# Performance work log

Measured on AMD Instinct MI355X. Metric: run time of the kernel, lower is better.

Reference implementation:

```python
import jax, jax.numpy as jnp
import numpy as np

B, S, IN, E, H, NH = 32, 1024, 16, 128, 256, 4
DH = E // NH
EPS = 1e-5


def _ln(x, g, b):
    mu = jnp.mean(x, axis=-1, keepdims=True)
    var = jnp.mean(jnp.square(x - mu), axis=-1, keepdims=True)
    return (x - mu) * jax.lax.rsqrt(var + EPS) * g + b


def setup_inputs() -> dict:
    key = jax.random.key(0)
    ks = iter(jax.random.split(key, 32))
    n = lambda shape, s=0.02: jax.random.normal(next(ks), shape, jnp.float32) * s
    inp = {
        "x": jax.random.normal(next(ks), (B, S, IN), jnp.float32),
        "mask": jax.random.uniform(next(ks), (B, S), jnp.float32),
        "embed_w": n((E, IN)), "embed_b": jnp.zeros((E,), jnp.float32),
        # 3 encoder layers, params stacked on leading layer axis
        "in_proj_w": n((3, 3 * E, E)), "in_proj_b": jnp.zeros((3, 3 * E), jnp.float32),
        "out_w": n((3, E, E)), "out_b": jnp.zeros((3, E), jnp.float32),
        "ln1_g": jnp.ones((3, E), jnp.float32), "ln1_b": jnp.zeros((3, E), jnp.float32),
        "ln2_g": jnp.ones((3, E), jnp.float32), "ln2_b": jnp.zeros((3, E), jnp.float32),
        "ffn_w1": n((3, E, E)), "ffn_b1": jnp.zeros((3, E), jnp.float32),
        "ffn_w2": n((3, E, E)), "ffn_b2": jnp.zeros((3, E), jnp.float32),
        "cls_w1": n((H, E)), "cls_b1": jnp.zeros((H,), jnp.float32),
        "cls_w2": n((H, H)), "cls_b2": jnp.zeros((H,), jnp.float32),
        "cls_w3": n((H, H)), "cls_b3": jnp.zeros((H,), jnp.float32),
        "cls_w4": n((1, H)), "cls_b4": jnp.zeros((1,), jnp.float32),
    }
    return inp


def _encoder_layer(x, ipw, ipb, ow, ob, g1, b1, g2, b2, w1, fb1, w2, fb2):
    # PyTorch TransformerEncoderLayer, norm_first=False (post-norm), relu FFN
    qkv = x @ ipw.T + ipb                      # [B,S,3E]
    q, k, v = jnp.split(qkv, 3, axis=-1)
    q = q.reshape(B, S, NH, DH).transpose(0, 2, 1, 3)
    k = k.reshape(B, S, NH, DH).transpose(0, 2, 1, 3)
    v = v.reshape(B, S, NH, DH).transpose(0, 2, 1, 3)
    scores = jnp.einsum("bhqd,bhkd->bhqk", q, k) / np.sqrt(DH)  # naive O(S^2) math SDPA
    attn = jax.nn.softmax(scores, axis=-1)
    o = jnp.einsum("bhqk,bhkd->bhqd", attn, v)
    o = o.transpose(0, 2, 1, 3).reshape(B, S, E) @ ow.T + ob
    x = _ln(x + o, g1, b1)
    ff = jax.nn.relu(x @ w1.T + fb1) @ w2.T + fb2
    return _ln(x + ff, g2, b2)


def reference(x, mask, embed_w, embed_b, in_proj_w, in_proj_b, out_w, out_b,
              ln1_g, ln1_b, ln2_g, ln2_b, ffn_w1, ffn_b1, ffn_w2, ffn_b2,
              cls_w1, cls_b1, cls_w2, cls_b2, cls_w3, cls_b3, cls_w4, cls_b4):
    h = jax.nn.relu(x @ embed_w.T + embed_b)   # [B,S,E]
    for i in range(3):
        h = _encoder_layer(h, in_proj_w[i], in_proj_b[i], out_w[i], out_b[i],
                           ln1_g[i], ln1_b[i], ln2_g[i], ln2_b[i],
                           ffn_w1[i], ffn_b1[i], ffn_w2[i], ffn_b2[i])
    pooled = jnp.sum(h * mask[:, :, None], axis=1)  # [B,E] masked sum pool
    z = jax.nn.relu(pooled @ cls_w1.T + cls_b1)
    z = jax.nn.relu(z @ cls_w2.T + cls_b2)
    z = jax.nn.relu(z @ cls_w3.T + cls_b3)
    return jax.nn.sigmoid(z @ cls_w4.T + cls_b4)    # [B,1]
```

## Files before the change

### kernel.cpp

```cpp
#include <hip/hip_runtime.h>
#include <hip/hip_bf16.h>
#include <math.h>

#define B 32
#define S 1024
#define IN_DIM 16
#define E 128
#define NH 4
#define DH 32
#define HDIM 256
#define ROWS (B*S)
#define EPS 1e-5f

#define N_IPW (3*384*128)
#define N_SQ  (3*128*128)
#define NCVT ((N_IPW + 3*N_SQ) / 256)

typedef __bf16 bf16x8 __attribute__((ext_vector_type(8)));
typedef __bf16 bf16x4 __attribute__((ext_vector_type(4)));
typedef __bf16 bf16x2 __attribute__((ext_vector_type(2)));
typedef float f32x4 __attribute__((ext_vector_type(4)));
typedef float f32x16 __attribute__((ext_vector_type(16)));

#define MFMA16 __builtin_amdgcn_mfma_f32_16x16x32_bf16
#define MFMA32 __builtin_amdgcn_mfma_f32_32x32x16_bf16

union BF2U { bf16x2 b; unsigned int u; };
__device__ inline unsigned int pk2(float a, float b) {
    BF2U x; x.b[0] = (__bf16)a; x.b[1] = (__bf16)b; return x.u;
}

union U8 { bf16x8 v8; bf16x4 v4[2]; unsigned u4[4]; };
__device__ inline void st8(__bf16* p, bf16x8 v) {
    U8 u; u.v8 = v;
    *(bf16x4*)p = u.v4[0];
    *(bf16x4*)(p + 4) = u.v4[1];
}
__device__ inline bf16x8 ld8(const __bf16* p) {
    U8 u;
    u.v4[0] = *(const bf16x4*)p;
    u.v4[1] = *(const bf16x4*)(p + 4);
    return u.v8;
}

__global__ __launch_bounds__(256) void k_embedcvt(
        const float* __restrict__ ipw, const float* __restrict__ ow,
        const float* __restrict__ w1, const float* __restrict__ w2,
        __bf16* __restrict__ wbo,
        const float* __restrict__ x, const float* __restrict__ W,
        const float* __restrict__ bias, __bf16* __restrict__ hb)
{
    int t = threadIdx.x;
    if (blockIdx.x < NCVT) {
        int i = blockIdx.x * 256 + t;
        float v;
        if (i < N_IPW) v = ipw[i];
        else if (i < N_IPW + N_SQ) v = ow[i - N_IPW];
        else if (i < N_IPW + 2 * N_SQ) v = w1[i - N_IPW - N_SQ];
        else v = w2[i - N_IPW - 2 * N_SQ];
        wbo[i] = (__bf16)v;
        return;
    }
    int row0 = (blockIdx.x - NCVT) * 16;
    __shared__ float xs[16][16];
    xs[t >> 4][t & 15] = x[(row0 + (t >> 4)) * IN_DIM + (t & 15)];
    __syncthreads();
    int sub = t >> 7, tc = t & 127;
    float w[16];
#pragma unroll
    for (int i = 0; i < 16; ++i) w[i] = W[tc * 16 + i];
    float bb = bias[tc];
#pragma unroll
    for (int rr = 0; rr < 8; ++rr) {
        int lr = sub * 8 + rr;
        float acc = bb;
#pragma unroll
        for (int i = 0; i < 16; ++i) acc += xs[lr][i] * w[i];
        hb[(size_t)(row0 + lr) * E + tc] = (__bf16)fmaxf(acc, 0.f);
    }
}

__global__ __launch_bounds__(512, 2) void k_qkvattn(
        const __bf16* __restrict__ hb, const __bf16* __restrict__ Wip,
        const float* __restrict__ bip, __bf16* __restrict__ O)
{
    __shared__ __attribute__((aligned(16))) __bf16 Ksh[1024][36];
    __shared__ __attribute__((aligned(16))) __bf16 Vsh[32][1036];
    __shared__ float lscr[8][64];

    int t = threadIdx.x, lane = t & 63, wv = t >> 6;
    int l15 = lane & 15, quad = lane >> 4;
    int l31 = lane & 31, hi = lane >> 5;
    int lb = ((blockIdx.x & 7) << 5) | (blockIdx.x >> 3);
    int half = lb & 1, bh = lb >> 1;
    int hh = bh & 3, b = bh >> 2;

    const __bf16* hpanel = hb + (size_t)b * S * E;

    const float qscale = 0.1767766952966369f * 1.4426950408889634f * 8388608.0f;
    const float C2 = 1065101558.0f;
    f32x16 cinit16, z16;
#pragma unroll
    for (int i = 0; i < 16; ++i) { cinit16[i] = C2; z16[i] = 0.f; }

    bf16x8 bQ[2][2];
    {
        bf16x8 bWq[8];
#pragma unroll
        for (int ch = 0; ch < 8; ++ch)
            bWq[ch] = *(const bf16x8*)&Wip[(size_t)(hh*32 + l31)*128 + ch*16 + hi*8];
        float bq = bip[hh*32 + l31];
#pragma unroll
        for (int qt = 0; qt < 2; ++qt) {
            int qrow0 = half*512 + wv*64 + qt*32;
            f32x16 aq = z16;
#pragma unroll
            for (int ch = 0; ch < 8; ++ch) {
                bf16x8 ah = *(const bf16x8*)&hpanel[(size_t)(qrow0 + l31)*128 + ch*16 + hi*8];
                aq = MFMA32(ah, bWq[ch], aq, 0, 0, 0);
            }
            __bf16* PmS = &Ksh[wv*128 + qt*32][0];
#pragma unroll
            for (int r = 0; r < 16; ++r) {
                int q = (r & 3) + 8*(r >> 2) + 4*hi;
                PmS[q*36 + l31] = (__bf16)((aq[r] + bq) * qscale);
            }
        }
        __asm__ __volatile__("" ::: "memory");
#pragma unroll
        for (int qt = 0; qt < 2; ++qt) {
            const __bf16* PmS = &Ksh[wv*128 + qt*32][0];
            bQ[qt][0] = ld8(&PmS[l31*36 + hi*8]);
            bQ[qt][1] = ld8(&PmS[l31*36 + 16 + hi*8]);
        }
        __asm__ __volatile__("" ::: "memory");
    }
    __syncthreads();

    {
        bf16x8 bWk[2][4], bWv[2][4];
#pragma unroll
        for (int df = 0; df < 2; ++df)
#pragma unroll
            for (int kc = 0; kc < 4; ++kc) {
                bWk[df][kc] = *(const bf16x8*)&Wip[(size_t)(128 + hh*32 + df*16 + l15)*128 + kc*32 + quad*8];
                bWv[df][kc] = *(const bf16x8*)&Wip[(size_t)(256 + hh*32 + df*16 + l15)*128 + kc*32 + quad*8];
            }
        float bk0 = bip[128 + hh*32 + l15],  bk1 = bip[128 + hh*32 + 16 + l15];
        float bvb0 = bip[256 + hh*32 + l15], bvb1 = bip[256 + hh*32 + 16 + l15];
        int srow = wv*16 + l15;
        bf16x8 af[4], ag[4];
#pragma unroll
        for (int kc = 0; kc < 4; ++kc)
            af[kc] = *(const bf16x8*)&hpanel[(size_t)srow*128 + kc*32 + quad*8];
        const f32x4 z4 = {0.f, 0.f, 0.f, 0.f};
        for (int c = 0; c < 8; ++c) {
            if (c < 7) {
#pragma unroll
                for (int kc = 0; kc < 4; ++kc)
                    ag[kc] = *(const bf16x8*)&hpanel[(size_t)((c+1)*128 + srow)*128 + kc*32 + quad*8];
            }
            f32x4 k0 = z4, k1 = z4, v0 = z4, v1 = z4;
#pragma unroll
            for (int kc = 0; kc < 4; ++kc) {
                k0 = MFMA16(af[kc], bWk[0][kc], k0, 0, 0, 0);
                k1 = MFMA16(af[kc], bWk[1][kc], k1, 0, 0, 0);
                v0 = MFMA16(af[kc], bWv[0][kc], v0, 0, 0, 0);
                v1 = MFMA16(af[kc], bWv[1][kc], v1, 0, 0, 0);
            }
            int s0 = c*128 + wv*16 + quad*4;
#pragma unroll
            for (int r = 0; r < 4; ++r) {
                Ksh[s0 + r][l15]      = (__bf16)(k0[r] + bk0);
                Ksh[s0 + r][16 + l15] = (__bf16)(k1[r] + bk1);
            }
            uint2 u0, u1;
            u0.x = pk2(v0[0] + bvb0, v0[1] + bvb0);
            u0.y = pk2(v0[2] + bvb0, v0[3] + bvb0);
            u1.x = pk2(v1[0] + bvb1, v1[1] + bvb1);
            u1.y = pk2(v1[2] + bvb1, v1[3] + bvb1);
            *(uint2*)&Vsh[l15][s0] = u0;
            *(uint2*)&Vsh[16 + l15][s0] = u1;
#pragma unroll
            for (int kc = 0; kc < 4; ++kc) af[kc] = ag[kc];
        }
    }
    __syncthreads();

    f32x16 o[2];
    o[0] = z16; o[1] = z16;
    float lsum[2] = {0.f, 0.f};

    bf16x8 aK[2][2], bVf[4];
#pragma unroll
    for (int sub = 0; sub < 2; ++sub)
#pragma unroll
        for (int dh = 0; dh < 2; ++dh)
            aK[sub][dh] = ld8(&Ksh[sub*32 + l31][dh*16 + hi*8]);
#pragma unroll
    for (int ch = 0; ch < 4; ++ch) {
        U8 u;
        const __bf16* vp = &Vsh[l31][ch*16 + hi*4];
        u.v4[0] = *(const bf16x4*)vp;
        u.v4[1] = *(const bf16x4*)(vp + 8);
        bVf[ch] = u.v8;
    }

    for (int c = 0; c < 16; ++c) {
        bf16x8 aKn[2][2], bVn[4];
        if (c < 15) {
#pragma unroll
            for (int sub = 0; sub < 2; ++sub)
#pragma unroll
                for (int dh = 0; dh < 2; ++dh)
                    aKn[sub][dh] = ld8(&Ksh[(c+1)*64 + sub*32 + l31][dh*16 + hi*8]);
#pragma unroll
            for (int ch = 0; ch < 4; ++ch) {
                U8 u;
                const __bf16* vp = &Vsh[l31][(c+1)*64 + ch*16 + hi*4];
                u.v4[0] = *(const bf16x4*)vp;
                u.v4[1] = *(const bf16x4*)(vp + 8);
                bVn[ch] = u.v8;
            }
        }
#pragma unroll
        for (int qt = 0; qt < 2; ++qt) {
#pragma unroll
            for (int sub = 0; sub < 2; ++sub) {
                f32x16 acc = cinit16;
                acc = MFMA32(aK[sub][0], bQ[qt][0], acc, 0, 0, 0);
                acc = MFMA32(aK[sub][1], bQ[qt][1], acc, 0, 0, 0);
#pragma unroll
                for (int g = 0; g < 2; ++g) {
                    U8 u;
                    float ls = 0.f;
#pragma unroll
                    for (int r = 0; r < 4; ++r) {
                        int ia = (int)acc[g*8 + 2*r];
                        int ib = (int)acc[g*8 + 2*r + 1];
                        u.u4[r] = __builtin_amdgcn_perm((unsigned)ib, (unsigned)ia, 0x07060302u);
                        ls += __int_as_float(ia) + __int_as_float(ib);
                    }
                    lsum[qt] += ls;
                    o[qt] = MFMA32(u.v8, bVf[sub*2 + g], o[qt], 0, 0, 0);
                }
            }
        }
        if (c < 15) {
#pragma unroll
            for (int sub = 0; sub < 2; ++sub)
#pragma unroll
                for (int dh = 0; dh < 2; ++dh)
                    aK[sub][dh] = aKn[sub][dh];
#pragma unroll
            for (int ch = 0; ch < 4; ++ch) bVf[ch] = bVn[ch];
        }
    }

#pragma unroll
    for (int qt = 0; qt < 2; ++qt) {
        float ls = lsum[qt] + __shfl_xor(lsum[qt], 32);
        if (hi == 0) lscr[wv][qt*32 + l31] = 1.f / ls;
    }
    __asm__ __volatile__("" ::: "memory");
#pragma unroll
    for (int qt = 0; qt < 2; ++qt)
#pragma unroll
        for (int r = 0; r < 16; ++r) {
            int q = (r & 3) + 8*(r >> 2) + 4*hi;
            float li = lscr[wv][qt*32 + q];
            int row = half*512 + wv*64 + qt*32 + q;
            O[((size_t)(b * S) + row) * E + hh*32 + l31] = (__bf16)(o[qt][r] * li);
        }
}

__global__ __launch_bounds__(512, 2) void k_layer2(const __bf16* __restrict__ t0b,
        const __bf16* __restrict__ Wo, const float* __restrict__ ob,
        const float* __restrict__ g1, const float* __restrict__ bt1,
        const __bf16* __restrict__ W1, const float* __restrict__ b1v,
        const __bf16* __restrict__ W2, const float* __restrict__ b2v,
        const float* __restrict__ g2, const float* __restrict__ bt2,
        __bf16* __restrict__ hb)
{
    __shared__ __attribute__((aligned(16))) __bf16 As[64][132];
    __shared__ __attribute__((aligned(16))) __bf16 Ws[128][132];
    __shared__ float red[2][64][2];
    int t = threadIdx.x;
    int m0 = blockIdx.x * 64;
    int arow = t >> 3, acol = (t & 7) * 16;
    int wrow = t >> 2, wcol = (t & 3) * 32;
    {
        const __bf16* Ap = t0b + (size_t)(m0 + arow) * 128 + acol;
#pragma unroll
        for (int j = 0; j < 2; ++j)
            st8(&As[arow][acol + j * 8], *(const bf16x8*)&Ap[j * 8]);
        const __bf16* Wp = Wo + (size_t)wrow * 128 + wcol;
#pragma unroll
        for (int j = 0; j < 4; ++j)
            st8(&Ws[wrow][wcol + j * 8], *(const bf16x8*)&Wp[j * 8]);
    }
    __syncthreads();
    int lane = t & 63, wv = t >> 6;
    int l15 = lane & 15, quad = lane >> 4;
    int nh = wv & 1, mh = wv >> 1;
    f32x4 acc[4];

#pragma unroll
    for (int i = 0; i < 4; ++i) acc[i] = (f32x4){0.f, 0.f, 0.f, 0.f};
#pragma unroll
    for (int kc = 0; kc < 4; ++kc) {
        bf16x8 aw[4], ba;
#pragma unroll
        for (int nc = 0; nc < 4; ++nc)
            aw[nc] = ld8(&Ws[nh * 64 + nc * 16 + l15][kc * 32 + quad * 8]);
        ba = ld8(&As[mh * 16 + l15][kc * 32 + quad * 8]);
#pragma unroll
        for (int nc = 0; nc < 4; ++nc)
            acc[nc] = MFMA16(aw[nc], ba, acc[nc], 0, 0, 0);
    }
    float s1 = 0.f, s2 = 0.f;
    int m = m0 + mh * 16 + l15;
#pragma unroll
    for (int nc = 0; nc < 4; ++nc) {
        float4 bv = *(const float4*)&ob[nh * 64 + nc * 16 + quad * 4];
        bf16x4 rv = *(const bf16x4*)&hb[(size_t)m * 128 + nh * 64 + nc * 16 + quad * 4];
        acc[nc][0] += bv.x + (float)rv[0];
        acc[nc][1] += bv.y + (float)rv[1];
        acc[nc][2] += bv.z + (float)rv[2];
        acc[nc][3] += bv.w + (float)rv[3];
#pragma unroll
        for (int i = 0; i < 4; ++i) {
            s1 += acc[nc][i];
            s2 += acc[nc][i] * acc[nc][i];
        }
    }
    s1 += __shfl_xor(s1, 16); s1 += __shfl_xor(s1, 32);
    s2 += __shfl_xor(s2, 16); s2 += __shfl_xor(s2, 32);
    if (quad == 0) {
        red[nh][mh * 16 + l15][0] = s1;
        red[nh][mh * 16 + l15][1] = s2;
    }
    __syncthreads();
    float mu, rs;
    {
        int r = mh * 16 + l15;
        float S1 = red[0][r][0] + red[1][r][0];
        float S2 = red[0][r][1] + red[1][r][1];
        mu = S1 * (1.f / 128.f);
        float var = S2 * (1.f / 128.f) - mu * mu;
        rs = rsqrtf(var + EPS);
    }
    bf16x4 res2[4];
#pragma unroll
    for (int nc = 0; nc < 4; ++nc) {
        float4 gv = *(const float4*)&g1[nh * 64 + nc * 16 + quad * 4];
        float4 bb = *(const float4*)&bt1[nh * 64 + nc * 16 + quad * 4];
        float o0 = (acc[nc][0] - mu) * rs * gv.x + bb.x;
        float o1 = (acc[nc][1] - mu) * rs * gv.y + bb.y;
        float o2 = (acc[nc][2] - mu) * rs * gv.z + bb.z;
        float o3 = (acc[nc][3] - mu) * rs * gv.w + bb.w;
        bf16x4 xb;
        xb[0] = (__bf16)o0; xb[1] = (__bf16)o1;
        xb[2] = (__bf16)o2; xb[3] = (__bf16)o3;
        res2[nc] = xb;
        *(bf16x4*)&As[mh * 16 + l15][nh * 64 + nc * 16 + quad * 4] = xb;
    }
    {
        const __bf16* Wp = W1 + (size_t)wrow * 128 + wcol;
#pragma unroll
        for (int j = 0; j < 4; ++j)
            st8(&Ws[wrow][wcol + j * 8], *(const bf16x8*)&Wp[j * 8]);
    }
    __syncthreads();

#pragma unroll
    for (int i = 0; i < 4; ++i) acc[i] = (f32x4){0.f, 0.f, 0.f, 0.f};
#pragma unroll
    for (int kc = 0; kc < 4; ++kc) {
        bf16x8 aw[4], ba;
#pragma unroll
        for (int nc = 0; nc < 4; ++nc)
            aw[nc] = ld8(&Ws[nh * 64 + nc * 16 + l15][kc * 32 + quad * 8]);
        ba = ld8(&As[mh * 16 + l15][kc * 32 + quad * 8]);
#pragma unroll
        for (int nc = 0; nc < 4; ++nc)
            acc[nc] = MFMA16(aw[nc], ba, acc[nc], 0, 0, 0);
    }
    __syncthreads();
#pragma unroll
    for (int nc = 0; nc < 4; ++nc) {
        float4 bv = *(const float4*)&b1v[nh * 64 + nc * 16 + quad * 4];
        float v0 = fmaxf(acc[nc][0] + bv.x, 0.f);
        float v1 = fmaxf(acc[nc][1] + bv.y, 0.f);
        float v2 = fmaxf(acc[nc][2] + bv.z, 0.f);
        float v3 = fmaxf(acc[nc][3] + bv.w, 0.f);
        uint2 u; u.x = pk2(v0, v1); u.y = pk2(v2, v3);
        *(uint2*)&As[mh * 16 + l15][nh * 64 + nc * 16 + quad * 4] = u;
    }
    {
        const __bf16* Wp = W2 + (size_t)wrow * 128 + wcol;
#pragma unroll
        for (int j = 0; j < 4; ++j)
            st8(&Ws[wrow][wcol + j * 8], *(const bf16x8*)&Wp[j * 8]);
    }
    __syncthreads();

#pragma unroll
    for (int i = 0; i < 4; ++i) acc[i] = (f32x4){0.f, 0.f, 0.f, 0.f};
#pragma unroll
    for (int kc = 0; kc < 4; ++kc) {
        bf16x8 aw[4], ba;
#pragma unroll
        for (int nc = 0; nc < 4; ++nc)
            aw[nc] = ld8(&Ws[nh * 64 + nc * 16 + l15][kc * 32 + quad * 8]);
        ba = ld8(&As[mh * 16 + l15][kc * 32 + quad * 8]);
#pragma unroll
        for (int nc = 0; nc < 4; ++nc)
            acc[nc] = MFMA16(aw[nc], ba, acc[nc], 0, 0, 0);
    }
    s1 = 0.f; s2 = 0.f;
#pragma unroll
    for (int nc = 0; nc < 4; ++nc) {
        float4 bv = *(const float4*)&b2v[nh * 64 + nc * 16 + quad * 4];
        acc[nc][0] += bv.x + (float)res2[nc][0];
        acc[nc][1] += bv.y + (float)res2[nc][1];
        acc[nc][2] += bv.z + (float)res2[nc][2];
        acc[nc][3] += bv.w + (float)res2[nc][3];
#pragma unroll
        for (int i = 0; i < 4; ++i) {
            s1 += acc[nc][i];
            s2 += acc[nc][i] * acc[nc][i];
        }
    }
    s1 += __shfl_xor(s1, 16); s1 += __shfl_xor(s1, 32);
    s2 += __shfl_xor(s2, 16); s2 += __shfl_xor(s2, 32);
    if (quad == 0) {
        red[nh][mh * 16 + l15][0] = s1;
        red[nh][mh * 16 + l15][1] = s2;
    }
    __syncthreads();
    {
        int r = mh * 16 + l15;
        float S1 = red[0][r][0] + red[1][r][0];
        float S2 = red[0][r][1] + red[1][r][1];
        mu = S1 * (1.f / 128.f);
        float var = S2 * (1.f / 128.f) - mu * mu;
        rs = rsqrtf(var + EPS);
    }
#pragma unroll
    for (int nc = 0; nc < 4; ++nc) {
        float4 gv = *(const float4*)&g2[nh * 64 + nc * 16 + quad * 4];
        float4 bb = *(const float4*)&bt2[nh * 64 + nc * 16 + quad * 4];
        float o0 = (acc[nc][0] - mu) * rs * gv.x + bb.x;
        float o1 = (acc[nc][1] - mu) * rs * gv.y + bb.y;
        float o2 = (acc[nc][2] - mu) * rs * gv.z + bb.z;
        float o3 = (acc[nc][3] - mu) * rs * gv.w + bb.w;
        uint2 u; u.x = pk2(o0, o1); u.y = pk2(o2, o3);
        *(uint2*)&hb[(size_t)m * 128 + nh * 64 + nc * 16 + quad * 4] = u;
    }
}

__global__ __launch_bounds__(256) void k_pool1(const __bf16* __restrict__ h,
        const float* __restrict__ mask, float* __restrict__ part)
{
    int bx = blockIdx.x;
    int b = bx >> 3, ch = bx & 7, t = threadIdx.x;
    int sg = t >> 4, cg = t & 15;
    __shared__ float red[16][128];
    float acc[8];
#pragma unroll
    for (int j = 0; j < 8; ++j) acc[j] = 0.f;
    const __bf16* hp = h + ((size_t)(b * S + ch * 128 + sg)) * E + cg * 8;
    const float* mp = mask + b * S + ch * 128 + sg;
#pragma unroll
    for (int k = 0; k < 8; ++k) {
        float m = mp[k * 16];
        bf16x8 hv = *(const bf16x8*)&hp[(size_t)(k * 16) * E];
#pragma unroll
        for (int j = 0; j < 8; ++j) acc[j] += (float)hv[j] * m;
    }
#pragma unroll
    for (int j = 0; j < 8; ++j) red[sg][cg * 8 + j] = acc[j];
    __syncthreads();
    if (t < 128) {
        float a = 0.f;
#pragma unroll
        for (int sgi = 0; sgi < 16; ++sgi) a += red[sgi][t];
        part[(size_t)bx * E + t] = a;
    }
}

__global__ __launch_bounds__(256) void k_head(const float* __restrict__ part,
        const float* __restrict__ cw1, const float* __restrict__ cb1,
        const float* __restrict__ cw2, const float* __restrict__ cb2,
        const float* __restrict__ cw3, const float* __restrict__ cb3,
        const float* __restrict__ cw4, const float* __restrict__ cb4,
        float* __restrict__ out)
{
    int b = blockIdx.x, t = threadIdx.x;
    __shared__ float p[128], za[256], zb[256];
    __shared__ float red4[4];
    if (t < 128) {
        float a = 0.f;
#pragma unroll
        for (int c = 0; c < 8; ++c) a += part[(size_t)(b * 8 + c) * 128 + t];
        p[t] = a;
    }
    __syncthreads();
    float a1 = cb1[t];
    for (int k = 0; k < 128; ++k) a1 += p[k] * cw1[t * 128 + k];
    za[t] = fmaxf(a1, 0.f);
    __syncthreads();
    float a2 = cb2[t];
    for (int k = 0; k < 256; ++k) a2 += za[k] * cw2[t * 256 + k];
    zb[t] = fmaxf(a2, 0.f);
    __syncthreads();
    float a3 = cb3[t];
    for (int k = 0; k < 256; ++k) a3 += zb[k] * cw3[t * 256 + k];
    float z3 = fmaxf(a3, 0.f);
    float prt = z3 * cw4[t];
#pragma unroll
    for (int o2 = 32; o2; o2 >>= 1) prt += __shfl_xor(prt, o2);
    if ((t & 63) == 0) red4[t >> 6] = prt;
    __syncthreads();
    if (t == 0) {
        float sum = red4[0] + red4[1] + red4[2] + red4[3] + cb4[0];
        out[b] = 1.f / (1.f + __expf(-sum));
    }
}

extern "C" void kernel_launch(void* const* d_in, const int* in_sizes, int n_in,
                              void* d_out, int out_size, void* d_ws, size_t ws_size,
                              hipStream_t stream)
{
    const float* x     = (const float*)d_in[0];
    const float* mask  = (const float*)d_in[1];
    const float* emb_w = (const float*)d_in[2];
    const float* emb_b = (const float*)d_in[3];
    const float* ipw   = (const float*)d_in[4];
    const float* ipb   = (const float*)d_in[5];
    const float* ow    = (const float*)d_in[6];
    const float* ob    = (const float*)d_in[7];
    const float* ln1g  = (const float*)d_in[8];
    const float* ln1b  = (const float*)d_in[9];
    const float* ln2g  = (const float*)d_in[10];
    const float* ln2b  = (const float*)d_in[11];
    const float* w1    = (const float*)d_in[12];
    const float* fb1   = (const float*)d_in[13];
    const float* w2    = (const float*)d_in[14];
    const float* fb2   = (const float*)d_in[15];
    const float* cw1   = (const float*)d_in[16];
    const float* cb1   = (const float*)d_in[17];
    const float* cw2   = (const float*)d_in[18];
    const float* cb2   = (const float*)d_in[19];
    const float* cw3   = (const float*)d_in[20];
    const float* cb3   = (const float*)d_in[21];
    const float* cw4   = (const float*)d_in[22];
    const float* cb4   = (const float*)d_in[23];

    char* p = (char*)d_ws;
    __bf16* hb   = (__bf16*)p;   p += (size_t)ROWS * E * 2;
    p += (size_t)ROWS * 256 * 2;
    p += (size_t)ROWS * 32 * 4 * 2 / 4;
    __bf16* t0b  = (__bf16*)p;   p += (size_t)ROWS * E * 2;
    __bf16* wb   = (__bf16*)p;   p += (size_t)(N_IPW + 3 * N_SQ) * 2;
    float* part  = (float*)p;    p += (size_t)B * 8 * E * 4;

    __bf16* wb_ipw = wb;
    __bf16* wb_ow  = wb + N_IPW;
    __bf16* wb_w1  = wb_ow + N_SQ;
    __bf16* wb_w2  = wb_w1 + N_SQ;

    k_embedcvt<<<NCVT + ROWS / 16, 256, 0, stream>>>(
        ipw, ow, w1, w2, wb, x, emb_w, emb_b, hb);
    for (int L = 0; L < 3; ++L) {
        k_qkvattn<<<B * NH * 2, 512, 0, stream>>>(
            hb, wb_ipw + (size_t)L * 384 * 128, ipb + L * 384, t0b);
        k_layer2<<<ROWS / 64, 512, 0, stream>>>(
            t0b, wb_ow + (size_t)L * 128 * 128, ob + L * 128,
            ln1g + L * E, ln1b + L * E,
            wb_w1 + (size_t)L * 128 * 128, fb1 + L * 128,
            wb_w2 + (size_t)L * 128 * 128, fb2 + L * 128,
            ln2g + L * E, ln2b + L * E, hb);
    }
    k_pool1<<<B * 8, 256, 0, stream>>>(hb, mask, part);
    k_head<<<B, 256, 0, stream>>>(part, cw1, cb1, cw2, cb2, cw3, cb3, cw4, cb4,
                                  (float*)d_out);
}
```

Before: 296.5 us.

## Fuse masked pooling into final layer2 epilogue, vectorize head, stage embed weights

Removes the separate pooling kernel by computing masked per-block partial sums in the last layer's LayerNorm epilogue, using shuffles and shared memory, and writing 16 partials per batch. The head kernel now reduces 16 partials and uses float4 loads for its matvecs. The embed kernel stages the embedding weight in padded shared memory so global loads are coalesced. The aim is to save one launch and one re-read of the hidden state, at the cost of extra shuffles and a sync in layer2 on the final layer.

```diff
diff --git a/kernel.cpp b/kernel.cpp
--- a/kernel.cpp
+++ b/kernel.cpp
@@ -63,12 +63,18 @@
     }
     int row0 = (blockIdx.x - NCVT) * 16;
     __shared__ float xs[16][16];
+    __shared__ float wsh[128][17];
     xs[t >> 4][t & 15] = x[(row0 + (t >> 4)) * IN_DIM + (t & 15)];
+#pragma unroll
+    for (int j = 0; j < 8; ++j) {
+        int n = t * 8 + j;
+        wsh[n >> 4][n & 15] = W[n];
+    }
     __syncthreads();
     int sub = t >> 7, tc = t & 127;
     float w[16];
 #pragma unroll
-    for (int i = 0; i < 16; ++i) w[i] = W[tc * 16 + i];
+    for (int i = 0; i < 16; ++i) w[i] = wsh[tc][i];
     float bb = bias[tc];
 #pragma unroll
     for (int rr = 0; rr < 8; ++rr) {
@@ -280,11 +286,13 @@
         const __bf16* __restrict__ W1, const float* __restrict__ b1v,
         const __bf16* __restrict__ W2, const float* __restrict__ b2v,
         const float* __restrict__ g2, const float* __restrict__ bt2,
-        __bf16* __restrict__ hb)
+        __bf16* __restrict__ hb,
+        const float* __restrict__ mask, float* __restrict__ part, int doPool)
 {
     __shared__ __attribute__((aligned(16))) __bf16 As[64][132];
     __shared__ __attribute__((aligned(16))) __bf16 Ws[128][132];
     __shared__ float red[2][64][2];
+    __shared__ float psum[4][128];
     int t = threadIdx.x;
     int m0 = blockIdx.x * 64;
     int arow = t >> 3, acol = (t & 7) * 16;
@@ -447,6 +455,8 @@
         float var = S2 * (1.f / 128.f) - mu * mu;
         rs = rsqrtf(var + EPS);
     }
+    float pv[16];
+    float mk = doPool ? mask[m] : 0.f;
 #pragma unroll
     for (int nc = 0; nc < 4; ++nc) {
         float4 gv = *(const float4*)&g2[nh * 64 + nc * 16 + quad * 4];
@@ -457,36 +467,28 @@
         float o3 = (acc[nc][3] - mu) * rs * gv.w + bb.w;
         uint2 u; u.x = pk2(o0, o1); u.y = pk2(o2, o3);
         *(uint2*)&hb[(size_t)m * 128 + nh * 64 + nc * 16 + quad * 4] = u;
-    }
-}
-
-__global__ __launch_bounds__(256) void k_pool1(const __bf16* __restrict__ h,
-        const float* __restrict__ mask, float* __restrict__ part)
-{
-    int bx = blockIdx.x;
-    int b = bx >> 3, ch = bx & 7, t = threadIdx.x;
-    int sg = t >> 4, cg = t & 15;
-    __shared__ float red[16][128];
-    float acc[8];
-#pragma unroll
-    for (int j = 0; j < 8; ++j) acc[j] = 0.f;
-    const __bf16* hp = h + ((size_t)(b * S + ch * 128 + sg)) * E + cg * 8;
-    const float* mp = mask + b * S + ch * 128 + sg;
-#pragma unroll
-    for (int k = 0; k < 8; ++k) {
-        float m = mp[k * 16];
-        bf16x8 hv = *(const bf16x8*)&hp[(size_t)(k * 16) * E];
-#pragma unroll
-        for (int j = 0; j < 8; ++j) acc[j] += (float)hv[j] * m;
-    }
-#pragma unroll
-    for (int j = 0; j < 8; ++j) red[sg][cg * 8 + j] = acc[j];
-    __syncthreads();
-    if (t < 128) {
-        float a = 0.f;
-#pragma unroll
-        for (int sgi = 0; sgi < 16; ++sgi) a += red[sgi][t];
-        part[(size_t)bx * E + t] = a;
+        pv[nc*4 + 0] = o0 * mk; pv[nc*4 + 1] = o1 * mk;
+        pv[nc*4 + 2] = o2 * mk; pv[nc*4 + 3] = o3 * mk;
+    }
+    if (doPool) {
+#pragma unroll
+        for (int j = 0; j < 16; ++j) {
+            float v = pv[j];
+            v += __shfl_xor(v, 1); v += __shfl_xor(v, 2);
+            v += __shfl_xor(v, 4); v += __shfl_xor(v, 8);
+            pv[j] = v;
+        }
+        if (l15 == 0) {
+#pragma unroll
+            for (int nc = 0; nc < 4; ++nc)
+#pragma unroll
+                for (int i = 0; i < 4; ++i)
+                    psum[mh][nh * 64 + nc * 16 + quad * 4 + i] = pv[nc*4 + i];
+        }
+        __syncthreads();
+        if (t < 128)
+            part[(size_t)blockIdx.x * 128 + t] =
+                psum[0][t] + psum[1][t] + psum[2][t] + psum[3][t];
     }
 }
 
@@ -498,25 +500,47 @@
         float* __restrict__ out)
 {
     int b = blockIdx.x, t = threadIdx.x;
-    __shared__ float p[128], za[256], zb[256];
+    __shared__ __attribute__((aligned(16))) float p[128];
+    __shared__ __attribute__((aligned(16))) float za[256], zb[256];
     __shared__ float red4[4];
     if (t < 128) {
         float a = 0.f;
 #pragma unroll
-        for (int c = 0; c < 8; ++c) a += part[(size_t)(b * 8 + c) * 128 + t];
+        for (int c = 0; c < 16; ++c) a += part[(size_t)(b * 16 + c) * 128 + t];
         p[t] = a;
     }
     __syncthreads();
     float a1 = cb1[t];
-    for (int k = 0; k < 128; ++k) a1 += p[k] * cw1[t * 128 + k];
+    {
+        const float4* pw = (const float4*)&cw1[t * 128];
+        const float4* pp = (const float4*)p;
+        for (int k = 0; k < 32; ++k) {
+            float4 w4 = pw[k], p4 = pp[k];
+            a1 += p4.x * w4.x + p4.y * w4.y + p4.z * w4.z + p4.w * w4.w;
+        }
+    }
     za[t] = fmaxf(a1, 0.f);
     __syncthreads();
     float a2 = cb2[t];
-    for (int k = 0; k < 256; ++k) a2 += za[k] * cw2[t * 256 + k];
+    {
+        const float4* pw = (const float4*)&cw2[t * 256];
+        const float4* pp = (const float4*)za;
+        for (int k = 0; k < 64; ++k) {
+            float4 w4 = pw[k], p4 = pp[k];
+            a2 += p4.x * w4.x + p4.y * w4.y + p4.z * w4.z + p4.w * w4.w;
+        }
+    }
     zb[t] = fmaxf(a2, 0.f);
     __syncthreads();
     float a3 = cb3[t];
-    for (int k = 0; k < 256; ++k) a3 += zb[k] * cw3[t * 256 + k];
+    {
+        const float4* pw = (const float4*)&cw3[t * 256];
+        const float4* pp = (const float4*)zb;
+        for (int k = 0; k < 64; ++k) {
+            float4 w4 = pw[k], p4 = pp[k];
+            a3 += p4.x * w4.x + p4.y * w4.y + p4.z * w4.z + p4.w * w4.w;
+        }
+    }
     float z3 = fmaxf(a3, 0.f);
     float prt = z3 * cw4[t];
 #pragma unroll
@@ -564,7 +588,7 @@
     p += (size_t)ROWS * 32 * 4 * 2 / 4;
     __bf16* t0b  = (__bf16*)p;   p += (size_t)ROWS * E * 2;
     __bf16* wb   = (__bf16*)p;   p += (size_t)(N_IPW + 3 * N_SQ) * 2;
-    float* part  = (float*)p;    p += (size_t)B * 8 * E * 4;
+    float* part  = (float*)p;    p += (size_t)(ROWS / 64) * E * 4;
 
     __bf16* wb_ipw = wb;
     __bf16* wb_ow  = wb + N_IPW;
@@ -581,9 +605,9 @@
             ln1g + L * E, ln1b + L * E,
             wb_w1 + (size_t)L * 128 * 128, fb1 + L * 128,
             wb_w2 + (size_t)L * 128 * 128, fb2 + L * 128,
-            ln2g + L * E, ln2b + L * E, hb);
-    }
-    k_pool1<<<B * 8, 256, 0, stream>>>(hb, mask, part);
+            ln2g + L * E, ln2b + L * E, hb,
+            mask, part, (L == 2) ? 1 : 0);
+    }
     k_head<<<B, 256, 0, stream>>>(part, cw1, cb1, cw2, cb2, cw3, cb3, cw4, cb4,
                                   (float*)d_out);
 }
```

Result: no change. 299.2 us (+0.9%).
